# Kernel optimization log

Hardware: AMD Instinct MI355X
Metric: run time of the kernel (lower is better)

## Reference

```python
import jax, jax.numpy as jnp
import numpy as np

B, L, D, H, DFF = 16, 2048, 256, 8, 1024
CYCLES = 2
DEP = D // H
EPS = 1e-6


def _mha(q, k, v, Wq, Wk, Wv, Wo, bo):
    # q: [N, Lq, D], k/v: [N, Lk, D]  (mask is None in the source for both calls)
    N, Lq, _ = q.shape
    Lk = k.shape[1]
    qh = (q @ Wq).reshape(N, Lq, H, DEP)
    kh = (k @ Wk).reshape(N, Lk, H, DEP)
    vh = (v @ Wv).reshape(N, Lk, H, DEP)
    logits = jnp.einsum('nqhd,nkhd->nhqk', qh, kh) / jnp.sqrt(jnp.float32(DEP))
    w = jax.nn.softmax(logits, axis=-1)
    o = jnp.einsum('nhqk,nkhd->nqhd', w, vh).reshape(N, Lq, D)
    return o @ Wo + bo


def _layernorm(x, g, b):
    mu = jnp.mean(x, axis=-1, keepdims=True)
    var = jnp.mean(jnp.square(x - mu), axis=-1, keepdims=True)
    return g * (x - mu) * jax.lax.rsqrt(var + EPS) + b


def setup_inputs() -> dict:
    key = jax.random.key(0)
    ks = jax.random.split(key, 10)
    sc = 1.0 / np.sqrt(D)
    return {
        'e': jax.random.normal(ks[0], (B, L, D), dtype=jnp.float32),
        'Wq': jax.random.normal(ks[1], (D, D), dtype=jnp.float32) * sc,
        'Wk': jax.random.normal(ks[2], (D, D), dtype=jnp.float32) * sc,
        'Wv': jax.random.normal(ks[3], (D, D), dtype=jnp.float32) * sc,
        'Wo': jax.random.normal(ks[4], (D, D), dtype=jnp.float32) * sc,
        'bo': jnp.zeros((D,), dtype=jnp.float32),
        'W1': jax.random.normal(ks[5], (D, DFF), dtype=jnp.float32) * sc,
        'b1': jnp.zeros((DFF,), dtype=jnp.float32),
        'W2': jax.random.normal(ks[6], (DFF, D), dtype=jnp.float32) * (1.0 / np.sqrt(DFF)),
        'b2': jnp.zeros((D,), dtype=jnp.float32),
        'g1': jnp.ones((D,), dtype=jnp.float32),
        'be1': jnp.zeros((D,), dtype=jnp.float32),
        'g2': jnp.ones((D,), dtype=jnp.float32),
        'be2': jnp.zeros((D,), dtype=jnp.float32),
        'training': False,
    }


def reference(e, Wq, Wk, Wv, Wo, bo, W1, b1, W2, b2, g1, be1, g2, be2, training):
    # training=False -> dropouts are identity (eval mode)
    b, l, d = e.shape
    h = e
    s = jnp.mean(h, axis=1)  # relay node [b, d]
    for _ in range(CYCLES):
        h_last = jnp.roll(h, -1, axis=1)  # cycle_shift(h, False)
        h_next = jnp.roll(h, 1, axis=1)   # cycle_shift(h, True)
        s_m = jnp.broadcast_to(s[:, None, :], h.shape)
        # context [b, l, 5, d] -> [b*l, 5, d]
        c = jnp.stack([h_last, h, h_next, e, s_m], axis=-2).reshape(b * l, 5, d)
        hq = h.reshape(b * l, 1, d)
        h = jax.nn.relu(_mha(hq, c, c, Wq, Wk, Wv, Wo, bo)).reshape(b, l, d)
        # relay attention (the source reuses multi_att_satellite weights here)
        sq = s[:, None, :]               # [b, 1, d]
        mc = jnp.concatenate([sq, h], axis=1)  # [b, l+1, d]
        s = jax.nn.relu(_mha(sq, mc, mc, Wq, Wk, Wv, Wo, bo)).reshape(b, d)
    out1 = _layernorm(e + h, g1, be1)
    ffn = jax.nn.relu(out1 @ W1 + b1) @ W2 + b2
    out2 = _layernorm(out1 + ffn, g2, be2)
    return out2, s
```

## Files before the change

kernel.cpp:

```cpp
#include <hip/hip_runtime.h>

typedef unsigned short u16;
typedef unsigned int u32;
typedef __attribute__((ext_vector_type(8))) short bf16x8;
typedef __attribute__((ext_vector_type(4))) float f32x4;

#define LCONST __launch_bounds__(256)

__device__ __forceinline__ u16 f2bf(float f) {
  u32 u = __float_as_uint(f);
  u32 r = (u + 0x7FFFu + ((u >> 16) & 1u)) >> 16;
  return (u16)r;
}
__device__ __forceinline__ float bflo(u32 w) { return __uint_as_float(w << 16); }
__device__ __forceinline__ float bfhi(u32 w) { return __uint_as_float(w & 0xFFFF0000u); }
__device__ __forceinline__ float b2f(u16 v) { return __uint_as_float(((u32)v) << 16); }

__device__ __forceinline__ float dot8(uint4 u, const float* q) {
  return q[0]*bflo(u.x) + q[1]*bfhi(u.x) + q[2]*bflo(u.y) + q[3]*bfhi(u.y)
       + q[4]*bflo(u.z) + q[5]*bfhi(u.z) + q[6]*bflo(u.w) + q[7]*bfhi(u.w);
}
__device__ __forceinline__ void fma8(uint4 u, float wt, float* a) {
  a[0] = fmaf(wt, bflo(u.x), a[0]); a[1] = fmaf(wt, bfhi(u.x), a[1]);
  a[2] = fmaf(wt, bflo(u.y), a[2]); a[3] = fmaf(wt, bfhi(u.y), a[3]);
  a[4] = fmaf(wt, bflo(u.z), a[4]); a[5] = fmaf(wt, bfhi(u.z), a[5]);
  a[6] = fmaf(wt, bflo(u.w), a[6]); a[7] = fmaf(wt, bfhi(u.w), a[7]);
}

__device__ __forceinline__ void gload16(const u16* g, u16* l) {
  __builtin_amdgcn_global_load_lds(
      (const __attribute__((address_space(1))) unsigned int*)g,
      (__attribute__((address_space(3))) unsigned int*)l, 16, 0, 0);
}

__global__ LCONST void prep_kernel(const float* __restrict__ e,
                                   const float* __restrict__ Wq, const float* __restrict__ Wk,
                                   const float* __restrict__ Wv, const float* __restrict__ Wo,
                                   const float* __restrict__ W1, const float* __restrict__ W2,
                                   u16* __restrict__ Wqkv_t, u16* __restrict__ Wo_t,
                                   u16* __restrict__ W1_t, u16* __restrict__ W2_t,
                                   float* __restrict__ part, u16* __restrict__ ebf) {
  int blk = blockIdx.x;
  int tid = threadIdx.x;
  if (blk < 3072) {
    int idx = blk * 256 + tid;
    if (idx < 196608) {
      int sub = idx >> 16, r = idx & 65535;
      int n = r >> 8, k = r & 255;
      const float* src = (sub == 0) ? Wq : ((sub == 1) ? Wk : Wv);
      Wqkv_t[idx] = f2bf(src[(size_t)k * 256 + n]);
    } else if (idx < 262144) {
      int r = idx - 196608;
      int n = r >> 8, k = r & 255;
      Wo_t[r] = f2bf(Wo[(size_t)k * 256 + n]);
    } else if (idx < 524288) {
      int r = idx - 262144;
      int n = r >> 8, k = r & 255;
      W1_t[r] = f2bf(W1[(size_t)k * 1024 + n]);
    } else {
      int r = idx - 524288;
      int n = r >> 10, k = r & 1023;
      W2_t[r] = f2bf(W2[(size_t)k * 256 + n]);
    }
  } else {
    int mb = blk - 3072;
    int b = mb >> 5, c = mb & 31;
    size_t base = ((size_t)b * 2048 + (size_t)c * 64) * 256 + tid;
    float s = 0.f;
    #pragma unroll 8
    for (int i = 0; i < 64; i++) {
      float v = e[base + (size_t)i * 256];
      s += v;
      ebf[base + (size_t)i * 256] = f2bf(v);
    }
    part[(size_t)mb * 256 + tid] = s;
  }
}

template <int BM, int BN, int EPI>
__global__ __launch_bounds__(512, (BM == 128) ? 4 : 6)
void gemm3_kernel(const u16* __restrict__ A, const u16* __restrict__ Bt,
                  const float* __restrict__ bias,
                  u16* __restrict__ C0, u16* __restrict__ C1, u16* __restrict__ C2,
                  const u16* __restrict__ resbf,
                  const float* __restrict__ g, const float* __restrict__ be,
                  float* __restrict__ Fout,
                  int M, int N, int K) {
  constexpr int WR = BM / 2;
  constexpr int MR = WR / 16;
  constexpr int ACH_PW = (BM / 8) / 8;
  constexpr int BCH_PW = 4;
  __shared__ __align__(16) u16 As[BM * 64];
  __shared__ __align__(16) u16 Bs[BN * 64];

  const int tid = threadIdx.x, lane = tid & 63, wid = tid >> 6;
  const int wm = wid >> 2, wn = wid & 3;

  const int ncol = N / BN;
  const int nwg = gridDim.x;
  const int bid = blockIdx.x;
  const int swz = (bid & 7) * (nwg >> 3) + (bid >> 3);
  const int mb = swz / ncol, nb = swz - mb * ncol;
  const int m0 = mb * BM, n0 = nb * BN;

  const int lrow8 = lane >> 3;
  const int cg = (lane & 7) ^ lrow8;

  f32x4 acc[MR][4] = {};
  for (int kt = 0; kt < K; kt += 64) {
    #pragma unroll
    for (int it = 0; it < ACH_PW; it++) {
      int ca = wid * ACH_PW + it;
      int row = ca * 8 + lrow8;
      gload16(A + (size_t)(m0 + row) * K + kt + cg * 8, (u16*)As + ca * 512);
    }
    #pragma unroll
    for (int it = 0; it < BCH_PW; it++) {
      int cb = wid * BCH_PW + it;
      int row = cb * 8 + lrow8;
      gload16(Bt + (size_t)(n0 + row) * K + kt + cg * 8, (u16*)Bs + cb * 512);
    }
    __syncthreads();
    const int lr = lane & 15, hi = lane >> 4;
    #pragma unroll
    for (int kk = 0; kk < 2; kk++) {
      const int slot = (kk * 4 + hi) ^ (lr & 7);
      bf16x8 af[MR], bfr[4];
      #pragma unroll
      for (int m = 0; m < MR; m++)
        af[m] = *(const bf16x8*)&As[(wm * WR + m * 16 + lr) * 64 + slot * 8];
      #pragma unroll
      for (int n = 0; n < 4; n++)
        bfr[n] = *(const bf16x8*)&Bs[(wn * 64 + n * 16 + lr) * 64 + slot * 8];
      #pragma unroll
      for (int m = 0; m < MR; m++)
        #pragma unroll
        for (int n = 0; n < 4; n++)
          acc[m][n] = __builtin_amdgcn_mfma_f32_16x16x32_bf16(af[m], bfr[n], acc[m][n], 0, 0, 0);
    }
    __syncthreads();
  }

  const int lr = lane & 15, hi = lane >> 4;
  if constexpr (EPI == 0) {
    const int bsel = n0 >> 8;
    u16* C = (bsel == 0) ? C0 : ((bsel == 1) ? C1 : C2);
    #pragma unroll
    for (int m = 0; m < MR; m++)
      #pragma unroll
      for (int n = 0; n < 4; n++)
        #pragma unroll
        for (int r = 0; r < 4; r++) {
          int row = m0 + wm * WR + m * 16 + hi * 4 + r;
          int col = wn * 64 + n * 16 + lr;
          C[(size_t)row * 256 + col] = f2bf(acc[m][n][r]);
        }
  } else if constexpr (EPI == 1) {
    #pragma unroll
    for (int m = 0; m < MR; m++)
      #pragma unroll
      for (int n = 0; n < 4; n++)
        #pragma unroll
        for (int r = 0; r < 4; r++) {
          int row = m0 + wm * WR + m * 16 + hi * 4 + r;
          int col = n0 + wn * 64 + n * 16 + lr;
          float v = fmaxf(acc[m][n][r] + bias[col], 0.f);
          C0[(size_t)row * N + col] = f2bf(v);
        }
  } else {
    __shared__ float rsum[BM], rsq[BM];
    if (tid < BM) { rsum[tid] = 0.f; rsq[tid] = 0.f; }
    __syncthreads();
    #pragma unroll
    for (int m = 0; m < MR; m++)
      #pragma unroll
      for (int n = 0; n < 4; n++)
        #pragma unroll
        for (int r = 0; r < 4; r++) {
          int rl = wm * WR + m * 16 + hi * 4 + r;
          int col = wn * 64 + n * 16 + lr;
          size_t gi = (size_t)(m0 + rl) * 256 + col;
          acc[m][n][r] = acc[m][n][r] + bias[col] + b2f(resbf[gi]);
        }
    #pragma unroll
    for (int m = 0; m < MR; m++)
      #pragma unroll
      for (int r = 0; r < 4; r++) {
        float s = 0.f, q = 0.f;
        #pragma unroll
        for (int n = 0; n < 4; n++) { float x = acc[m][n][r]; s += x; q += x * x; }
        #pragma unroll
        for (int off = 1; off < 16; off <<= 1) {
          s += __shfl_xor(s, off);
          q += __shfl_xor(q, off);
        }
        if (lr == 0) {
          int rl = wm * WR + m * 16 + hi * 4 + r;
          atomicAdd(&rsum[rl], s);
          atomicAdd(&rsq[rl], q);
        }
      }
    __syncthreads();
    #pragma unroll
    for (int m = 0; m < MR; m++)
      #pragma unroll
      for (int n = 0; n < 4; n++)
        #pragma unroll
        for (int r = 0; r < 4; r++) {
          int rl = wm * WR + m * 16 + hi * 4 + r;
          int col = wn * 64 + n * 16 + lr;
          size_t gi = (size_t)(m0 + rl) * 256 + col;
          float mu = rsum[rl] * (1.f / 256.f);
          float var = rsq[rl] * (1.f / 256.f) - mu * mu;
          float rstd = rsqrtf(fmaxf(var, 0.f) + 1e-6f);
          Fout[gi] = g[col] * (acc[m][n][r] - mu) * rstd + be[col];
        }
  }
}

template <int EPI>
__global__ __launch_bounds__(512, 4)
void attnwo_kernel(const u16* __restrict__ hq, const u16* __restrict__ pk,
                   const u16* __restrict__ pv, const u16* __restrict__ ek,
                   const u16* __restrict__ ev, const float* __restrict__ skp,
                   const float* __restrict__ svp,
                   const u16* __restrict__ Wo_t, const float* __restrict__ bo,
                   u16* __restrict__ C0, u16* __restrict__ C1,
                   const u16* __restrict__ resbf,
                   const float* __restrict__ g, const float* __restrict__ be) {
  __shared__ __align__(16) u16 As[64 * 256];
  __shared__ __align__(16) u16 Bs[256 * 64];
  const int tid = threadIdx.x, lane = tid & 63, wid = tid >> 6;
  const int wm = wid >> 2, wn = wid & 3;
  const int nwg = gridDim.x, bid = blockIdx.x;
  const int swz = (bid & 7) * (nwg >> 3) + (bid >> 3);
  const int m0 = swz * 64;

  {
    const int r = tid >> 3, h = tid & 7;
    const size_t token = (size_t)(m0 + r);
    const int b = (int)(token >> 11);
    const int i = (int)(token & 2047);
    const size_t tb = (size_t)b << 11;
    const size_t ip = tb + ((i + 1) & 2047);
    const size_t im = tb + ((i + 2047) & 2047);
    const int off = h * 32;

    float qf[32];
    {
      const u16* q = hq + token * 256 + off;
      #pragma unroll
      for (int c = 0; c < 4; c++) {
        uint4 u = *(const uint4*)(q + c * 8);
        qf[c*8+0] = bflo(u.x); qf[c*8+1] = bfhi(u.x);
        qf[c*8+2] = bflo(u.y); qf[c*8+3] = bfhi(u.y);
        qf[c*8+4] = bflo(u.z); qf[c*8+5] = bfhi(u.z);
        qf[c*8+6] = bflo(u.w); qf[c*8+7] = bfhi(u.w);
      }
    }
    const u16* kr0 = pk + ip * 256 + off;
    const u16* kr1 = pk + token * 256 + off;
    const u16* kr2 = pk + im * 256 + off;
    const u16* kr3 = ek + token * 256 + off;
    float lg[5];
    {
      float d0 = 0, d1 = 0, d2 = 0, d3 = 0;
      #pragma unroll
      for (int cc = 0; cc < 4; cc++) {
        d0 += dot8(*(const uint4*)(kr0 + cc * 8), qf + cc * 8);
        d1 += dot8(*(const uint4*)(kr1 + cc * 8), qf + cc * 8);
        d2 += dot8(*(const uint4*)(kr2 + cc * 8), qf + cc * 8);
        d3 += dot8(*(const uint4*)(kr3 + cc * 8), qf + cc * 8);
      }
      lg[0] = d0; lg[1] = d1; lg[2] = d2; lg[3] = d3;
      float d4 = 0;
      const float* s = skp + b * 256 + off;
      #pragma unroll
      for (int j = 0; j < 32; j++) d4 = fmaf(qf[j], s[j], d4);
      lg[4] = d4;
    }
    const float sc = 0.17677669529663687f;
    float mx = lg[0];
    #pragma unroll
    for (int c = 1; c < 5; c++) mx = fmaxf(mx, lg[c]);
    float w[5], den = 0.f;
    #pragma unroll
    for (int c = 0; c < 5; c++) { w[c] = __expf((lg[c] - mx) * sc); den += w[c]; }

    float a[32];
    #pragma unroll
    for (int j = 0; j < 32; j++) a[j] = 0.f;
    const u16* vr0 = pv + ip * 256 + off;
    const u16* vr1 = pv + token * 256 + off;
    const u16* vr2 = pv + im * 256 + off;
    const u16* vr3 = ev + token * 256 + off;
    #pragma unroll
    for (int cc = 0; cc < 4; cc++) {
      fma8(*(const uint4*)(vr0 + cc * 8), w[0], a + cc * 8);
      fma8(*(const uint4*)(vr1 + cc * 8), w[1], a + cc * 8);
      fma8(*(const uint4*)(vr2 + cc * 8), w[2], a + cc * 8);
      fma8(*(const uint4*)(vr3 + cc * 8), w[3], a + cc * 8);
    }
    {
      const float* s = svp + b * 256 + off;
      #pragma unroll
      for (int j = 0; j < 32; j++) a[j] = fmaf(w[4], s[j], a[j]);
    }
    const float inv = 1.f / den;
    #pragma unroll
    for (int c = 0; c < 4; c++) {
      uint4 u;
      u.x = (u32)f2bf(a[c*8+0] * inv) | ((u32)f2bf(a[c*8+1] * inv) << 16);
      u.y = (u32)f2bf(a[c*8+2] * inv) | ((u32)f2bf(a[c*8+3] * inv) << 16);
      u.z = (u32)f2bf(a[c*8+4] * inv) | ((u32)f2bf(a[c*8+5] * inv) << 16);
      u.w = (u32)f2bf(a[c*8+6] * inv) | ((u32)f2bf(a[c*8+7] * inv) << 16);
      int s = h * 4 + c;
      int sp = (s & 24) | ((s & 7) ^ (r & 7));
      *(uint4*)&As[r * 256 + sp * 8] = u;
    }
  }
  __syncthreads();

  const int lrow8 = lane >> 3;
  const int cg = (lane & 7) ^ lrow8;
  const int lr = lane & 15, hi = lane >> 4;
  f32x4 acc[2][4] = {};
  for (int kt = 0; kt < 4; kt++) {
    #pragma unroll
    for (int it = 0; it < 4; it++) {
      int cb = wid * 4 + it;
      int row = cb * 8 + lrow8;
      gload16(Wo_t + (size_t)row * 256 + kt * 64 + cg * 8, (u16*)Bs + cb * 512);
    }
    __syncthreads();
    #pragma unroll
    for (int kk = 0; kk < 2; kk++) {
      bf16x8 af[2], bfr[4];
      #pragma unroll
      for (int m = 0; m < 2; m++) {
        int row = wm * 32 + m * 16 + lr;
        int sp = kt * 8 + ((kk * 4 + hi) ^ (row & 7));
        af[m] = *(const bf16x8*)&As[row * 256 + sp * 8];
      }
      const int slotB = (kk * 4 + hi) ^ (lr & 7);
      #pragma unroll
      for (int n = 0; n < 4; n++)
        bfr[n] = *(const bf16x8*)&Bs[(wn * 64 + n * 16 + lr) * 64 + slotB * 8];
      #pragma unroll
      for (int m = 0; m < 2; m++)
        #pragma unroll
        for (int n = 0; n < 4; n++)
          acc[m][n] = __builtin_amdgcn_mfma_f32_16x16x32_bf16(af[m], bfr[n], acc[m][n], 0, 0, 0);
    }
    __syncthreads();
  }

  if constexpr (EPI == 1) {
    #pragma unroll
    for (int m = 0; m < 2; m++)
      #pragma unroll
      for (int n = 0; n < 4; n++)
        #pragma unroll
        for (int r = 0; r < 4; r++) {
          int row = m0 + wm * 32 + m * 16 + hi * 4 + r;
          int col = wn * 64 + n * 16 + lr;
          float v = fmaxf(acc[m][n][r] + bo[col], 0.f);
          C0[(size_t)row * 256 + col] = f2bf(v);
        }
  } else {
    __shared__ float rsum[64], rsq[64];
    if (tid < 64) { rsum[tid] = 0.f; rsq[tid] = 0.f; }
    __syncthreads();
    #pragma unroll
    for (int m = 0; m < 2; m++)
      #pragma unroll
      for (int n = 0; n < 4; n++)
        #pragma unroll
        for (int r = 0; r < 4; r++) {
          int rl = wm * 32 + m * 16 + hi * 4 + r;
          int col = wn * 64 + n * 16 + lr;
          size_t gi = (size_t)(m0 + rl) * 256 + col;
          float v = fmaxf(acc[m][n][r] + bo[col], 0.f);
          C0[gi] = f2bf(v);
          acc[m][n][r] = b2f(resbf[gi]) + v;
        }
    #pragma unroll
    for (int m = 0; m < 2; m++)
      #pragma unroll
      for (int r = 0; r < 4; r++) {
        float s = 0.f, q = 0.f;
        #pragma unroll
        for (int n = 0; n < 4; n++) { float x = acc[m][n][r]; s += x; q += x * x; }
        #pragma unroll
        for (int off = 1; off < 16; off <<= 1) {
          s += __shfl_xor(s, off);
          q += __shfl_xor(q, off);
        }
        if (lr == 0) {
          int rl = wm * 32 + m * 16 + hi * 4 + r;
          atomicAdd(&rsum[rl], s);
          atomicAdd(&rsq[rl], q);
        }
      }
    __syncthreads();
    #pragma unroll
    for (int m = 0; m < 2; m++)
      #pragma unroll
      for (int n = 0; n < 4; n++)
        #pragma unroll
        for (int r = 0; r < 4; r++) {
          int rl = wm * 32 + m * 16 + hi * 4 + r;
          int col = wn * 64 + n * 16 + lr;
          size_t gi = (size_t)(m0 + rl) * 256 + col;
          float mu = rsum[rl] * (1.f / 256.f);
          float var = rsq[rl] * (1.f / 256.f) - mu * mu;
          float rstd = rsqrtf(fmaxf(var, 0.f) + 1e-6f);
          C1[gi] = f2bf(g[col] * (acc[m][n][r] - mu) * rstd + be[col]);
        }
  }
}

template <bool MEAN>
__global__ LCONST void proj_kernel(const float* __restrict__ X, const float* __restrict__ part,
                                   const float* __restrict__ Wq, const float* __restrict__ Wk,
                                   const float* __restrict__ Wv, float* __restrict__ Yq,
                                   float* __restrict__ Yk, float* __restrict__ Yv) {
  __shared__ float xs[256];
  __shared__ float red[256];
  const int b = blockIdx.x;
  const int wsel = blockIdx.y >> 2, n0 = (blockIdx.y & 3) * 64;
  const int tid = threadIdx.x;
  if constexpr (MEAN) {
    float s = 0.f;
    #pragma unroll
    for (int c = 0; c < 32; c++) s += part[((size_t)b * 32 + c) * 256 + tid];
    xs[tid] = s * (1.f / 2048.f);
  } else {
    xs[tid] = X[b * 256 + tid];
  }
  __syncthreads();
  const float* W = (wsel == 0) ? Wq : ((wsel == 1) ? Wk : Wv);
  float* Y = (wsel == 0) ? Yq : ((wsel == 1) ? Yk : Yv);
  const int c = tid & 63, g = tid >> 6;
  float p = 0.f;
  #pragma unroll 8
  for (int j = g * 64; j < g * 64 + 64; j++)
    p = fmaf(xs[j], W[(size_t)j * 256 + n0 + c], p);
  red[tid] = p;
  __syncthreads();
  if (g == 0)
    Y[b * 256 + n0 + c] = red[c] + red[64 + c] + red[128 + c] + red[192 + c];
}

__global__ LCONST void mha2a_kernel(const float* __restrict__ sqp, const float* __restrict__ skp,
                                    const float* __restrict__ svp, const u16* __restrict__ pk,
                                    const u16* __restrict__ pv, float* __restrict__ partial) {
  __shared__ float rmax[4], rsum[4], racc[4][32];
  const int blk = blockIdx.x;
  const int bh = blk >> 2, c = blk & 3;
  const int b = bh >> 3, h = bh & 7;
  const int tid = threadIdx.x;
  const int lane = tid & 63, wid = tid >> 6;
  const int off = h * 32;
  const float sc = 0.17677669529663687f;

  float qf[32];
  {
    const float* q = sqp + b * 256 + off;
    #pragma unroll
    for (int j = 0; j < 32; j++) qf[j] = q[j];
  }
  const int k0 = c * 512 + tid;
  const int k1 = k0 + 256;
  const u16* kp0 = pk + ((size_t)b * 2048 + k0) * 256 + off;
  const u16* kp1 = pk + ((size_t)b * 2048 + k1) * 256 + off;
  float d0 = 0.f, d1 = 0.f;
  #pragma unroll
  for (int cc = 0; cc < 4; cc++) {
    d0 += dot8(*(const uint4*)(kp0 + cc * 8), qf + cc * 8);
    d1 += dot8(*(const uint4*)(kp1 + cc * 8), qf + cc * 8);
  }
  d0 *= sc; d1 *= sc;
  float ds = -1e30f;
  if (c == 0 && tid == 0) {
    float d = 0.f;
    const float* k = skp + b * 256 + off;
    #pragma unroll
    for (int j = 0; j < 32; j++) d = fmaf(qf[j], k[j], d);
    ds = d * sc;
  }
  float lmax = fmaxf(fmaxf(d0, d1), ds);
  #pragma unroll
  for (int o = 32; o; o >>= 1) lmax = fmaxf(lmax, __shfl_down(lmax, o));
  if (lane == 0) rmax[wid] = lmax;
  __syncthreads();
  const float M = fmaxf(fmaxf(rmax[0], rmax[1]), fmaxf(rmax[2], rmax[3]));

  float w0 = __expf(d0 - M), w1 = __expf(d1 - M);
  float lsum = w0 + w1;
  float a[32];
  #pragma unroll
  for (int j = 0; j < 32; j++) a[j] = 0.f;
  const u16* vp0 = pv + ((size_t)b * 2048 + k0) * 256 + off;
  const u16* vp1 = pv + ((size_t)b * 2048 + k1) * 256 + off;
  #pragma unroll
  for (int cc = 0; cc < 4; cc++) {
    fma8(*(const uint4*)(vp0 + cc * 8), w0, a + cc * 8);
    fma8(*(const uint4*)(vp1 + cc * 8), w1, a + cc * 8);
  }
  if (c == 0 && tid == 0) {
    float ws = __expf(ds - M);
    lsum += ws;
    const float* v = svp + b * 256 + off;
    #pragma unroll
    for (int j = 0; j < 32; j++) a[j] = fmaf(ws, v[j], a[j]);
  }
  #pragma unroll
  for (int o = 32; o; o >>= 1) lsum += __shfl_down(lsum, o);
  if (lane == 0) rsum[wid] = lsum;
  #pragma unroll
  for (int j = 0; j < 32; j++) {
    float v = a[j];
    #pragma unroll
    for (int o = 32; o; o >>= 1) v += __shfl_down(v, o);
    if (lane == 0) racc[wid][j] = v;
  }
  __syncthreads();
  float* P = partial + (size_t)blk * 36;
  if (tid < 32) {
    P[2 + tid] = racc[0][tid] + racc[1][tid] + racc[2][tid] + racc[3][tid];
    if (tid == 0) {
      P[0] = M;
      P[1] = rsum[0] + rsum[1] + rsum[2] + rsum[3];
    }
  }
}

__global__ LCONST void mha2c_kernel(const float* __restrict__ partial,
                                    const float* __restrict__ Wo, const float* __restrict__ bo,
                                    float* __restrict__ Y) {
  __shared__ float xs[256];
  __shared__ float red[256];
  const int b = blockIdx.x;
  const int n0 = blockIdx.y * 64;
  const int tid = threadIdx.x;
  {
    int hh = tid >> 5, d = tid & 31;
    const float* P = partial + (size_t)(b * 8 + hh) * 144;
    float M = fmaxf(fmaxf(P[0], P[36]), fmaxf(P[72], P[108]));
    float l = 0.f, o = 0.f;
    #pragma unroll
    for (int c = 0; c < 4; c++) {
      float f = __expf(P[c * 36] - M);
      l += f * P[c * 36 + 1];
      o += f * P[c * 36 + 2 + d];
    }
    xs[tid] = o / l;
  }
  __syncthreads();
  const int c = tid & 63, g = tid >> 6;
  float p = 0.f;
  #pragma unroll 8
  for (int j = g * 64; j < g * 64 + 64; j++)
    p = fmaf(xs[j], Wo[(size_t)j * 256 + n0 + c], p);
  red[tid] = p;
  __syncthreads();
  if (g == 0) {
    float v = red[c] + red[64 + c] + red[128 + c] + red[192 + c];
    Y[b * 256 + n0 + c] = fmaxf(v + bo[n0 + c], 0.f);
  }
}

extern "C" void kernel_launch(void* const* d_in, const int* in_sizes, int n_in,
                              void* d_out, int out_size, void* d_ws, size_t ws_size,
                              hipStream_t stream) {
  const float* e   = (const float*)d_in[0];
  const float* Wq  = (const float*)d_in[1];
  const float* Wk  = (const float*)d_in[2];
  const float* Wv  = (const float*)d_in[3];
  const float* Wo  = (const float*)d_in[4];
  const float* bo  = (const float*)d_in[5];
  const float* W1  = (const float*)d_in[6];
  const float* b1  = (const float*)d_in[7];
  const float* W2  = (const float*)d_in[8];
  const float* b2  = (const float*)d_in[9];
  const float* g1  = (const float*)d_in[10];
  const float* be1 = (const float*)d_in[11];
  const float* g2  = (const float*)d_in[12];
  const float* be2 = (const float*)d_in[13];

  char* wsb = (char*)d_ws;
  size_t off = 0;
  auto alc = [&](size_t n) { void* p = wsb + off; off += (n + 255) & ~(size_t)255; return p; };
  u16* Wqkv_t = (u16*)alc(768 * 256 * 2);
  u16* Wo_t   = (u16*)alc(65536 * 2);
  u16* W1_t   = (u16*)alc(262144 * 2);
  u16* W2_t   = (u16*)alc(262144 * 2);
  float* sB    = (float*)alc(4096 * 4);
  float* sqp   = (float*)alc(4096 * 4);
  float* skp   = (float*)alc(4096 * 4);
  float* svp   = (float*)alc(4096 * 4);
  float* partM = (float*)alc(512 * 36 * 4);
  float* part  = (float*)alc(524288);
  const size_t SZ = 16777216;
  u16* hq   = (u16*)alc(SZ);
  u16* ek   = (u16*)alc(SZ);
  u16* ev   = (u16*)alc(SZ);
  u16* pk   = (u16*)alc(SZ);
  u16* pv   = (u16*)alc(SZ);
  u16* hbuf = (u16*)alc(SZ);
  u16* ebf  = (u16*)alc(SZ);
  u16* out1 = (u16*)alc(SZ);
  u16* ffn1 = hq;

  const int M = 32768;
  float* outp  = (float*)d_out;
  float* s_out = outp + 8388608;

  prep_kernel<<<3584, 256, 0, stream>>>(e, Wq, Wk, Wv, Wo, W1, W2,
      Wqkv_t, Wo_t, W1_t, W2_t, part, ebf);

  proj_kernel<true><<<dim3(16, 12), 256, 0, stream>>>(nullptr, part, Wq, Wk, Wv, sqp, skp, svp);
  gemm3_kernel<128, 256, 0><<<768, 512, 0, stream>>>(ebf, Wqkv_t, nullptr, hq, ek, ev,
      nullptr, nullptr, nullptr, nullptr, M, 768, 256);
  attnwo_kernel<1><<<512, 512, 0, stream>>>(hq, ek, ev, ek, ev, skp, svp,
      Wo_t, bo, hbuf, nullptr, nullptr, nullptr, nullptr);
  gemm3_kernel<128, 256, 0><<<768, 512, 0, stream>>>(hbuf, Wqkv_t, nullptr, hq, pk, pv,
      nullptr, nullptr, nullptr, nullptr, M, 768, 256);
  mha2a_kernel<<<512, 256, 0, stream>>>(sqp, skp, svp, pk, pv, partM);
  mha2c_kernel<<<dim3(16, 4), 256, 0, stream>>>(partM, Wo, bo, sB);
  proj_kernel<false><<<dim3(16, 12), 256, 0, stream>>>(sB, nullptr, Wq, Wk, Wv, sqp, skp, svp);

  attnwo_kernel<2><<<512, 512, 0, stream>>>(hq, pk, pv, ek, ev, skp, svp,
      Wo_t, bo, hbuf, out1, ebf, g1, be1);
  gemm3_kernel<128, 256, 0><<<512, 512, 0, stream>>>(hbuf, Wqkv_t + 65536, nullptr, pk, pv, nullptr,
      nullptr, nullptr, nullptr, nullptr, M, 512, 256);
  mha2a_kernel<<<512, 256, 0, stream>>>(sqp, skp, svp, pk, pv, partM);
  mha2c_kernel<<<dim3(16, 4), 256, 0, stream>>>(partM, Wo, bo, s_out);

  gemm3_kernel<128, 256, 1><<<1024, 512, 0, stream>>>(out1, W1_t, b1, ffn1, nullptr, nullptr,
      nullptr, nullptr, nullptr, nullptr, M, 1024, 256);
  gemm3_kernel<64, 256, 4><<<512, 512, 0, stream>>>(ffn1, W2_t, b2, nullptr, nullptr, nullptr,
      out1, g2, be2, outp, M, 256, 1024);
  (void)in_sizes; (void)n_in; (void)out_size; (void)ws_size;
}
```

Baseline: 258.5 us.

## Merge independent GEMM and attention launches into horizontally fused kernels

Measured after the change: 262.8 us. About the same (+1.7%).

```diff
diff --git a/kernel.cpp b/kernel.cpp
--- a/kernel.cpp
+++ b/kernel.cpp
@@ -78,7 +78,144 @@
 }
 
 template <int BM, int BN, int EPI>
-__global__ __launch_bounds__(512, (BM == 128) ? 4 : 6)
+__device__ __forceinline__ void gemm_core(
+    int bid, int nwg, u16* As, u16* Bs,
+    const u16* __restrict__ A, const u16* __restrict__ Bt,
+    const float* __restrict__ bias,
+    u16* __restrict__ C0, u16* __restrict__ C1, u16* __restrict__ C2,
+    const u16* __restrict__ resbf,
+    const float* __restrict__ g, const float* __restrict__ be,
+    float* __restrict__ Fout, int N, int K) {
+  constexpr int WR = BM / 2;
+  constexpr int MR = WR / 16;
+  constexpr int ACH_PW = (BM / 8) / 8;
+  constexpr int BCH_PW = 4;
+
+  const int tid = threadIdx.x, lane = tid & 63, wid = tid >> 6;
+  const int wm = wid >> 2, wn = wid & 3;
+
+  const int ncol = N / BN;
+  const int swz = (bid & 7) * (nwg >> 3) + (bid >> 3);
+  const int mb = swz / ncol, nb = swz - mb * ncol;
+  const int m0 = mb * BM, n0 = nb * BN;
+
+  const int lrow8 = lane >> 3;
+  const int cg = (lane & 7) ^ lrow8;
+
+  f32x4 acc[MR][4] = {};
+  for (int kt = 0; kt < K; kt += 64) {
+    #pragma unroll
+    for (int it = 0; it < ACH_PW; it++) {
+      int ca = wid * ACH_PW + it;
+      int row = ca * 8 + lrow8;
+      gload16(A + (size_t)(m0 + row) * K + kt + cg * 8, As + ca * 512);
+    }
+    #pragma unroll
+    for (int it = 0; it < BCH_PW; it++) {
+      int cb = wid * BCH_PW + it;
+      int row = cb * 8 + lrow8;
+      gload16(Bt + (size_t)(n0 + row) * K + kt + cg * 8, Bs + cb * 512);
+    }
+    __syncthreads();
+    const int lr = lane & 15, hi = lane >> 4;
+    #pragma unroll
+    for (int kk = 0; kk < 2; kk++) {
+      const int slot = (kk * 4 + hi) ^ (lr & 7);
+      bf16x8 af[MR], bfr[4];
+      #pragma unroll
+      for (int m = 0; m < MR; m++)
+        af[m] = *(const bf16x8*)&As[(wm * WR + m * 16 + lr) * 64 + slot * 8];
+      #pragma unroll
+      for (int n = 0; n < 4; n++)
+        bfr[n] = *(const bf16x8*)&Bs[(wn * 64 + n * 16 + lr) * 64 + slot * 8];
+      #pragma unroll
+      for (int m = 0; m < MR; m++)
+        #pragma unroll
+        for (int n = 0; n < 4; n++)
+          acc[m][n] = __builtin_amdgcn_mfma_f32_16x16x32_bf16(af[m], bfr[n], acc[m][n], 0, 0, 0);
+    }
+    __syncthreads();
+  }
+
+  const int lr = lane & 15, hi = lane >> 4;
+  if constexpr (EPI == 0) {
+    const int bsel = n0 >> 8;
+    u16* C = (bsel == 0) ? C0 : ((bsel == 1) ? C1 : C2);
+    #pragma unroll
+    for (int m = 0; m < MR; m++)
+      #pragma unroll
+      for (int n = 0; n < 4; n++)
+        #pragma unroll
+        for (int r = 0; r < 4; r++) {
+          int row = m0 + wm * WR + m * 16 + hi * 4 + r;
+          int col = wn * 64 + n * 16 + lr;
+          C[(size_t)row * 256 + col] = f2bf(acc[m][n][r]);
+        }
+  } else if constexpr (EPI == 1) {
+    #pragma unroll
+    for (int m = 0; m < MR; m++)
+      #pragma unroll
+      for (int n = 0; n < 4; n++)
+        #pragma unroll
+        for (int r = 0; r < 4; r++) {
+          int row = m0 + wm * WR + m * 16 + hi * 4 + r;
+          int col = n0 + wn * 64 + n * 16 + lr;
+          float v = fmaxf(acc[m][n][r] + bias[col], 0.f);
+          C0[(size_t)row * N + col] = f2bf(v);
+        }
+  } else {
+    __shared__ float rs_[BM], rq_[BM];
+    if (tid < BM) { rs_[tid] = 0.f; rq_[tid] = 0.f; }
+    __syncthreads();
+    #pragma unroll
+    for (int m = 0; m < MR; m++)
+      #pragma unroll
+      for (int n = 0; n < 4; n++)
+        #pragma unroll
+        for (int r = 0; r < 4; r++) {
+          int rl = wm * WR + m * 16 + hi * 4 + r;
+          int col = wn * 64 + n * 16 + lr;
+          size_t gi = (size_t)(m0 + rl) * 256 + col;
+          acc[m][n][r] = acc[m][n][r] + bias[col] + b2f(resbf[gi]);
+        }
+    #pragma unroll
+    for (int m = 0; m < MR; m++)
+      #pragma unroll
+      for (int r = 0; r < 4; r++) {
+        float s = 0.f, q = 0.f;
+        #pragma unroll
+        for (int n = 0; n < 4; n++) { float x = acc[m][n][r]; s += x; q += x * x; }
+        #pragma unroll
+        for (int off = 1; off < 16; off <<= 1) {
+          s += __shfl_xor(s, off);
+          q += __shfl_xor(q, off);
+        }
+        if (lr == 0) {
+          int rl = wm * WR + m * 16 + hi * 4 + r;
+          atomicAdd(&rs_[rl], s);
+          atomicAdd(&rq_[rl], q);
+        }
+      }
+    __syncthreads();
+    #pragma unroll
+    for (int m = 0; m < MR; m++)
+      #pragma unroll
+      for (int n = 0; n < 4; n++)
+        #pragma unroll
+        for (int r = 0; r < 4; r++) {
+          int rl = wm * WR + m * 16 + hi * 4 + r;
+          int col = wn * 64 + n * 16 + lr;
+          size_t gi = (size_t)(m0 + rl) * 256 + col;
+          float mu = rs_[rl] * (1.f / 256.f);
+          float var = rq_[rl] * (1.f / 256.f) - mu * mu;
+          float rstd = rsqrtf(fmaxf(var, 0.f) + 1e-6f);
+          Fout[gi] = g[col] * (acc[m][n][r] - mu) * rstd + be[col];
+        }
+  }
+}
+
+template <int BM, int BN, int EPI>
+__global__ __launch_bounds__(512, 4)
 void gemm3_kernel(const u16* __restrict__ A, const u16* __restrict__ Bt,
                   const float* __restrict__ bias,
                   u16* __restrict__ C0, u16* __restrict__ C1, u16* __restrict__ C2,
@@ -86,136 +223,114 @@
                   const float* __restrict__ g, const float* __restrict__ be,
                   float* __restrict__ Fout,
                   int M, int N, int K) {
-  constexpr int WR = BM / 2;
-  constexpr int MR = WR / 16;
-  constexpr int ACH_PW = (BM / 8) / 8;
-  constexpr int BCH_PW = 4;
   __shared__ __align__(16) u16 As[BM * 64];
   __shared__ __align__(16) u16 Bs[BN * 64];
-
-  const int tid = threadIdx.x, lane = tid & 63, wid = tid >> 6;
-  const int wm = wid >> 2, wn = wid & 3;
-
-  const int ncol = N / BN;
-  const int nwg = gridDim.x;
-  const int bid = blockIdx.x;
-  const int swz = (bid & 7) * (nwg >> 3) + (bid >> 3);
-  const int mb = swz / ncol, nb = swz - mb * ncol;
-  const int m0 = mb * BM, n0 = nb * BN;
-
-  const int lrow8 = lane >> 3;
-  const int cg = (lane & 7) ^ lrow8;
-
-  f32x4 acc[MR][4] = {};
-  for (int kt = 0; kt < K; kt += 64) {
-    #pragma unroll
-    for (int it = 0; it < ACH_PW; it++) {
-      int ca = wid * ACH_PW + it;
-      int row = ca * 8 + lrow8;
-      gload16(A + (size_t)(m0 + row) * K + kt + cg * 8, (u16*)As + ca * 512);
-    }
-    #pragma unroll
-    for (int it = 0; it < BCH_PW; it++) {
-      int cb = wid * BCH_PW + it;
-      int row = cb * 8 + lrow8;
-      gload16(Bt + (size_t)(n0 + row) * K + kt + cg * 8, (u16*)Bs + cb * 512);
-    }
-    __syncthreads();
-    const int lr = lane & 15, hi = lane >> 4;
-    #pragma unroll
-    for (int kk = 0; kk < 2; kk++) {
-      const int slot = (kk * 4 + hi) ^ (lr & 7);
-      bf16x8 af[MR], bfr[4];
-      #pragma unroll
-      for (int m = 0; m < MR; m++)
-        af[m] = *(const bf16x8*)&As[(wm * WR + m * 16 + lr) * 64 + slot * 8];
-      #pragma unroll
-      for (int n = 0; n < 4; n++)
-        bfr[n] = *(const bf16x8*)&Bs[(wn * 64 + n * 16 + lr) * 64 + slot * 8];
-      #pragma unroll
-      for (int m = 0; m < MR; m++)
-        #pragma unroll
-        for (int n = 0; n < 4; n++)
-          acc[m][n] = __builtin_amdgcn_mfma_f32_16x16x32_bf16(af[m], bfr[n], acc[m][n], 0, 0, 0);
-    }
-    __syncthreads();
-  }
-
-  const int lr = lane & 15, hi = lane >> 4;
-  if constexpr (EPI == 0) {
-    const int bsel = n0 >> 8;
-    u16* C = (bsel == 0) ? C0 : ((bsel == 1) ? C1 : C2);
-    #pragma unroll
-    for (int m = 0; m < MR; m++)
-      #pragma unroll
-      for (int n = 0; n < 4; n++)
-        #pragma unroll
-        for (int r = 0; r < 4; r++) {
-          int row = m0 + wm * WR + m * 16 + hi * 4 + r;
-          int col = wn * 64 + n * 16 + lr;
-          C[(size_t)row * 256 + col] = f2bf(acc[m][n][r]);
-        }
-  } else if constexpr (EPI == 1) {
-    #pragma unroll
-    for (int m = 0; m < MR; m++)
-      #pragma unroll
-      for (int n = 0; n < 4; n++)
-        #pragma unroll
-        for (int r = 0; r < 4; r++) {
-          int row = m0 + wm * WR + m * 16 + hi * 4 + r;
-          int col = n0 + wn * 64 + n * 16 + lr;
-          float v = fmaxf(acc[m][n][r] + bias[col], 0.f);
-          C0[(size_t)row * N + col] = f2bf(v);
-        }
-  } else {
-    __shared__ float rsum[BM], rsq[BM];
-    if (tid < BM) { rsum[tid] = 0.f; rsq[tid] = 0.f; }
-    __syncthreads();
-    #pragma unroll
-    for (int m = 0; m < MR; m++)
-      #pragma unroll
-      for (int n = 0; n < 4; n++)
-        #pragma unroll
-        for (int r = 0; r < 4; r++) {
-          int rl = wm * WR + m * 16 + hi * 4 + r;
-          int col = wn * 64 + n * 16 + lr;
-          size_t gi = (size_t)(m0 + rl) * 256 + col;
-          acc[m][n][r] = acc[m][n][r] + bias[col] + b2f(resbf[gi]);
-        }
-    #pragma unroll
-    for (int m = 0; m < MR; m++)
-      #pragma unroll
-      for (int r = 0; r < 4; r++) {
-        float s = 0.f, q = 0.f;
-        #pragma unroll
-        for (int n = 0; n < 4; n++) { float x = acc[m][n][r]; s += x; q += x * x; }
-        #pragma unroll
-        for (int off = 1; off < 16; off <<= 1) {
-          s += __shfl_xor(s, off);
-          q += __shfl_xor(q, off);
-        }
-        if (lr == 0) {
-          int rl = wm * WR + m * 16 + hi * 4 + r;
-          atomicAdd(&rsum[rl], s);
-          atomicAdd(&rsq[rl], q);
-        }
-      }
-    __syncthreads();
-    #pragma unroll
-    for (int m = 0; m < MR; m++)
-      #pragma unroll
-      for (int n = 0; n < 4; n++)
-        #pragma unroll
-        for (int r = 0; r < 4; r++) {
-          int rl = wm * WR + m * 16 + hi * 4 + r;
-          int col = wn * 64 + n * 16 + lr;
-          size_t gi = (size_t)(m0 + rl) * 256 + col;
-          float mu = rsum[rl] * (1.f / 256.f);
-          float var = rsq[rl] * (1.f / 256.f) - mu * mu;
-          float rstd = rsqrtf(fmaxf(var, 0.f) + 1e-6f);
-          Fout[gi] = g[col] * (acc[m][n][r] - mu) * rstd + be[col];
-        }
-  }
+  gemm_core<BM, BN, EPI>(blockIdx.x, gridDim.x, As, Bs, A, Bt, bias,
+                         C0, C1, C2, resbf, g, be, Fout, N, K);
+  (void)M;
+}
+
+template <int NT>
+__device__ __forceinline__ void mha2a_body(int blk,
+    const float* __restrict__ sqp, const float* __restrict__ skp,
+    const float* __restrict__ svp, const u16* __restrict__ pk,
+    const u16* __restrict__ pv, float* __restrict__ partial) {
+  constexpr int NW = NT / 64;
+  constexpr int KPT = 512 / NT;
+  __shared__ float rmax[NW], rsm[NW], racc[NW][32];
+  const int bh = blk >> 2, c = blk & 3;
+  const int b = bh >> 3, h = bh & 7;
+  const int tid = threadIdx.x;
+  const int lane = tid & 63, wid = tid >> 6;
+  const int off = h * 32;
+  const float sc = 0.17677669529663687f;
+
+  float qf[32];
+  {
+    const float* q = sqp + b * 256 + off;
+    #pragma unroll
+    for (int j = 0; j < 32; j++) qf[j] = q[j];
+  }
+  float d[KPT];
+  #pragma unroll
+  for (int kk = 0; kk < KPT; kk++) {
+    int k = c * 512 + kk * NT + tid;
+    const u16* kp = pk + ((size_t)b * 2048 + k) * 256 + off;
+    float dv = 0.f;
+    #pragma unroll
+    for (int cc = 0; cc < 4; cc++) dv += dot8(*(const uint4*)(kp + cc * 8), qf + cc * 8);
+    d[kk] = dv * sc;
+  }
+  float ds = -1e30f;
+  if (c == 0 && tid == 0) {
+    float dv = 0.f;
+    const float* k = skp + b * 256 + off;
+    #pragma unroll
+    for (int j = 0; j < 32; j++) dv = fmaf(qf[j], k[j], dv);
+    ds = dv * sc;
+  }
+  float lmax = ds;
+  #pragma unroll
+  for (int kk = 0; kk < KPT; kk++) lmax = fmaxf(lmax, d[kk]);
+  #pragma unroll
+  for (int o = 32; o; o >>= 1) lmax = fmaxf(lmax, __shfl_down(lmax, o));
+  if (lane == 0) rmax[wid] = lmax;
+  __syncthreads();
+  float M = rmax[0];
+  #pragma unroll
+  for (int w = 1; w < NW; w++) M = fmaxf(M, rmax[w]);
+
+  float lsum = 0.f;
+  float a[32];
+  #pragma unroll
+  for (int j = 0; j < 32; j++) a[j] = 0.f;
+  #pragma unroll
+  for (int kk = 0; kk < KPT; kk++) {
+    int k = c * 512 + kk * NT + tid;
+    float wt = __expf(d[kk] - M);
+    lsum += wt;
+    const u16* vp = pv + ((size_t)b * 2048 + k) * 256 + off;
+    #pragma unroll
+    for (int cc = 0; cc < 4; cc++) fma8(*(const uint4*)(vp + cc * 8), wt, a + cc * 8);
+  }
+  if (c == 0 && tid == 0) {
+    float ws = __expf(ds - M);
+    lsum += ws;
+    const float* v = svp + b * 256 + off;
+    #pragma unroll
+    for (int j = 0; j < 32; j++) a[j] = fmaf(ws, v[j], a[j]);
+  }
+  #pragma unroll
+  for (int o = 32; o; o >>= 1) lsum += __shfl_down(lsum, o);
+  if (lane == 0) rsm[wid] = lsum;
+  #pragma unroll
+  for (int j = 0; j < 32; j++) {
+    float v = a[j];
+    #pragma unroll
+    for (int o = 32; o; o >>= 1) v += __shfl_down(v, o);
+    if (lane == 0) racc[wid][j] = v;
+  }
+  __syncthreads();
+  float* P = partial + (size_t)blk * 36;
+  if (tid < 32) {
+    float acc = 0.f;
+    #pragma unroll
+    for (int w = 0; w < NW; w++) acc += racc[w][tid];
+    P[2 + tid] = acc;
+    if (tid == 0) {
+      float l = 0.f;
+      #pragma unroll
+      for (int w = 0; w < NW; w++) l += rsm[w];
+      P[0] = M;
+      P[1] = l;
+    }
+  }
+}
+
+__global__ LCONST void mha2a_kernel(const float* __restrict__ sqp, const float* __restrict__ skp,
+                                    const float* __restrict__ svp, const u16* __restrict__ pk,
+                                    const u16* __restrict__ pv, float* __restrict__ partial) {
+  mha2a_body<256>(blockIdx.x, sqp, skp, svp, pk, pv, partial);
 }
 
 template <int EPI>
@@ -235,6 +350,15 @@
   const int nwg = gridDim.x, bid = blockIdx.x;
   const int swz = (bid & 7) * (nwg >> 3) + (bid >> 3);
   const int m0 = swz * 64;
+  const int lrow8 = lane >> 3;
+  const int cg = (lane & 7) ^ lrow8;
+
+  #pragma unroll
+  for (int it = 0; it < 4; it++) {
+    int cb = wid * 4 + it;
+    int row = cb * 8 + lrow8;
+    gload16(Wo_t + (size_t)row * 256 + 0 * 64 + cg * 8, (u16*)Bs + cb * 512);
+  }
 
   {
     const int r = tid >> 3, h = tid & 7;
@@ -321,18 +445,9 @@
   }
   __syncthreads();
 
-  const int lrow8 = lane >> 3;
-  const int cg = (lane & 7) ^ lrow8;
   const int lr = lane & 15, hi = lane >> 4;
   f32x4 acc[2][4] = {};
   for (int kt = 0; kt < 4; kt++) {
-    #pragma unroll
-    for (int it = 0; it < 4; it++) {
-      int cb = wid * 4 + it;
-      int row = cb * 8 + lrow8;
-      gload16(Wo_t + (size_t)row * 256 + kt * 64 + cg * 8, (u16*)Bs + cb * 512);
-    }
-    __syncthreads();
     #pragma unroll
     for (int kk = 0; kk < 2; kk++) {
       bf16x8 af[2], bfr[4];
@@ -353,6 +468,15 @@
           acc[m][n] = __builtin_amdgcn_mfma_f32_16x16x32_bf16(af[m], bfr[n], acc[m][n], 0, 0, 0);
     }
     __syncthreads();
+    if (kt < 3) {
+      #pragma unroll
+      for (int it = 0; it < 4; it++) {
+        int cb = wid * 4 + it;
+        int row = cb * 8 + lrow8;
+        gload16(Wo_t + (size_t)row * 256 + (kt + 1) * 64 + cg * 8, (u16*)Bs + cb * 512);
+      }
+      __syncthreads();
+    }
   }
 
   if constexpr (EPI == 1) {
@@ -452,87 +576,86 @@
     Y[b * 256 + n0 + c] = red[c] + red[64 + c] + red[128 + c] + red[192 + c];
 }
 
-__global__ LCONST void mha2a_kernel(const float* __restrict__ sqp, const float* __restrict__ skp,
-                                    const float* __restrict__ svp, const u16* __restrict__ pk,
-                                    const u16* __restrict__ pv, float* __restrict__ partial) {
-  __shared__ float rmax[4], rsum[4], racc[4][32];
-  const int blk = blockIdx.x;
-  const int bh = blk >> 2, c = blk & 3;
-  const int b = bh >> 3, h = bh & 7;
-  const int tid = threadIdx.x;
-  const int lane = tid & 63, wid = tid >> 6;
-  const int off = h * 32;
-  const float sc = 0.17677669529663687f;
-
-  float qf[32];
-  {
-    const float* q = sqp + b * 256 + off;
-    #pragma unroll
-    for (int j = 0; j < 32; j++) qf[j] = q[j];
-  }
-  const int k0 = c * 512 + tid;
-  const int k1 = k0 + 256;
-  const u16* kp0 = pk + ((size_t)b * 2048 + k0) * 256 + off;
-  const u16* kp1 = pk + ((size_t)b * 2048 + k1) * 256 + off;
-  float d0 = 0.f, d1 = 0.f;
-  #pragma unroll
-  for (int cc = 0; cc < 4; cc++) {
-    d0 += dot8(*(const uint4*)(kp0 + cc * 8), qf + cc * 8);
-    d1 += dot8(*(const uint4*)(kp1 + cc * 8), qf + cc * 8);
-  }
-  d0 *= sc; d1 *= sc;
-  float ds = -1e30f;
-  if (c == 0 && tid == 0) {
-    float d = 0.f;
-    const float* k = skp + b * 256 + off;
-    #pragma unroll
-    for (int j = 0; j < 32; j++) d = fmaf(qf[j], k[j], d);
-    ds = d * sc;
-  }
-  float lmax = fmaxf(fmaxf(d0, d1), ds);
-  #pragma unroll
-  for (int o = 32; o; o >>= 1) lmax = fmaxf(lmax, __shfl_down(lmax, o));
-  if (lane == 0) rmax[wid] = lmax;
-  __syncthreads();
-  const float M = fmaxf(fmaxf(rmax[0], rmax[1]), fmaxf(rmax[2], rmax[3]));
-
-  float w0 = __expf(d0 - M), w1 = __expf(d1 - M);
-  float lsum = w0 + w1;
-  float a[32];
-  #pragma unroll
-  for (int j = 0; j < 32; j++) a[j] = 0.f;
-  const u16* vp0 = pv + ((size_t)b * 2048 + k0) * 256 + off;
-  const u16* vp1 = pv + ((size_t)b * 2048 + k1) * 256 + off;
-  #pragma unroll
-  for (int cc = 0; cc < 4; cc++) {
-    fma8(*(const uint4*)(vp0 + cc * 8), w0, a + cc * 8);
-    fma8(*(const uint4*)(vp1 + cc * 8), w1, a + cc * 8);
-  }
-  if (c == 0 && tid == 0) {
-    float ws = __expf(ds - M);
-    lsum += ws;
-    const float* v = svp + b * 256 + off;
-    #pragma unroll
-    for (int j = 0; j < 32; j++) a[j] = fmaf(ws, v[j], a[j]);
-  }
-  #pragma unroll
-  for (int o = 32; o; o >>= 1) lsum += __shfl_down(lsum, o);
-  if (lane == 0) rsum[wid] = lsum;
-  #pragma unroll
-  for (int j = 0; j < 32; j++) {
-    float v = a[j];
-    #pragma unroll
-    for (int o = 32; o; o >>= 1) v += __shfl_down(v, o);
-    if (lane == 0) racc[wid][j] = v;
-  }
-  __syncthreads();
-  float* P = partial + (size_t)blk * 36;
-  if (tid < 32) {
-    P[2 + tid] = racc[0][tid] + racc[1][tid] + racc[2][tid] + racc[3][tid];
-    if (tid == 0) {
-      P[0] = M;
-      P[1] = rsum[0] + rsum[1] + rsum[2] + rsum[3];
-    }
+__global__ __launch_bounds__(512, 4)
+void qkvproj_kernel(const u16* __restrict__ ebf, const u16* __restrict__ Wqkv_t,
+                    u16* __restrict__ hq, u16* __restrict__ ek, u16* __restrict__ ev,
+                    const float* __restrict__ part,
+                    const float* __restrict__ Wq, const float* __restrict__ Wk,
+                    const float* __restrict__ Wv, float* __restrict__ Yq,
+                    float* __restrict__ Yk, float* __restrict__ Yv) {
+  extern __shared__ __align__(16) char smem[];
+  const int bid = blockIdx.x, tid = threadIdx.x;
+  if (bid < 768) {
+    u16* As = (u16*)smem;
+    u16* Bs = As + 128 * 64;
+    gemm_core<128, 256, 0>(bid, 768, As, Bs, ebf, Wqkv_t, nullptr,
+                           hq, ek, ev, nullptr, nullptr, nullptr, nullptr, 768, 256);
+  } else {
+    float* xs = (float*)smem;
+    float* red = xs + 256;
+    const int vb = bid - 768;
+    const int b = vb & 15, y = vb >> 4;
+    const int wsel = y >> 2, n0 = (y & 3) * 64;
+    if (tid < 256) {
+      float s = 0.f;
+      #pragma unroll
+      for (int c = 0; c < 32; c++) s += part[((size_t)b * 32 + c) * 256 + tid];
+      xs[tid] = s * (1.f / 2048.f);
+    }
+    __syncthreads();
+    const float* W = (wsel == 0) ? Wq : ((wsel == 1) ? Wk : Wv);
+    float* Y = (wsel == 0) ? Yq : ((wsel == 1) ? Yk : Yv);
+    const int c = tid & 63, g = tid >> 6;
+    float p = 0.f;
+    #pragma unroll 8
+    for (int j = g * 32; j < g * 32 + 32; j++)
+      p = fmaf(xs[j], W[(size_t)j * 256 + n0 + c], p);
+    red[tid] = p;
+    __syncthreads();
+    if (g == 0) {
+      float v = 0.f;
+      #pragma unroll
+      for (int k = 0; k < 8; k++) v += red[k * 64 + c];
+      Y[b * 256 + n0 + c] = v;
+    }
+  }
+}
+
+__global__ __launch_bounds__(512, 4)
+void kvffn_kernel(const u16* __restrict__ out1, const u16* __restrict__ W1_t,
+                  const float* __restrict__ b1, u16* __restrict__ ffn1,
+                  const u16* __restrict__ hbuf, const u16* __restrict__ Wkv_t,
+                  u16* __restrict__ pk, u16* __restrict__ pv) {
+  extern __shared__ __align__(16) char smem[];
+  u16* As = (u16*)smem;
+  u16* Bs = As + 128 * 64;
+  const int bid = blockIdx.x;
+  if (bid < 1024) {
+    gemm_core<128, 256, 1>(bid, 1024, As, Bs, out1, W1_t, b1,
+                           ffn1, nullptr, nullptr, nullptr, nullptr, nullptr, nullptr, 1024, 256);
+  } else {
+    gemm_core<128, 256, 0>(bid - 1024, 512, As, Bs, hbuf, Wkv_t, nullptr,
+                           pk, pv, nullptr, nullptr, nullptr, nullptr, nullptr, 512, 256);
+  }
+}
+
+__global__ __launch_bounds__(512, 4)
+void ffn2mha_kernel(const u16* __restrict__ ffn1, const u16* __restrict__ W2_t,
+                    const float* __restrict__ b2, const u16* __restrict__ out1,
+                    const float* __restrict__ g2, const float* __restrict__ be2,
+                    float* __restrict__ outp,
+                    const float* __restrict__ sqp, const float* __restrict__ skp,
+                    const float* __restrict__ svp, const u16* __restrict__ pk,
+                    const u16* __restrict__ pv, float* __restrict__ partial) {
+  extern __shared__ __align__(16) char smem[];
+  const int bid = blockIdx.x;
+  if (bid < 512) {
+    u16* As = (u16*)smem;
+    u16* Bs = As + 64 * 64;
+    gemm_core<64, 256, 4>(bid, 512, As, Bs, ffn1, W2_t, b2,
+                          nullptr, nullptr, nullptr, out1, g2, be2, outp, 256, 1024);
+  } else {
+    mha2a_body<512>(bid - 512, sqp, skp, svp, pk, pv, partial);
   }
 }
 
@@ -606,10 +729,10 @@
   u16* hq   = (u16*)alc(SZ);
   u16* ek   = (u16*)alc(SZ);
   u16* ev   = (u16*)alc(SZ);
+  u16* ebf  = (u16*)alc(SZ);
   u16* pk   = (u16*)alc(SZ);
   u16* pv   = (u16*)alc(SZ);
   u16* hbuf = (u16*)alc(SZ);
-  u16* ebf  = (u16*)alc(SZ);
   u16* out1 = (u16*)alc(SZ);
   u16* ffn1 = hq;
 
@@ -620,9 +743,8 @@
   prep_kernel<<<3584, 256, 0, stream>>>(e, Wq, Wk, Wv, Wo, W1, W2,
       Wqkv_t, Wo_t, W1_t, W2_t, part, ebf);
 
-  proj_kernel<true><<<dim3(16, 12), 256, 0, stream>>>(nullptr, part, Wq, Wk, Wv, sqp, skp, svp);
-  gemm3_kernel<128, 256, 0><<<768, 512, 0, stream>>>(ebf, Wqkv_t, nullptr, hq, ek, ev,
-      nullptr, nullptr, nullptr, nullptr, M, 768, 256);
+  qkvproj_kernel<<<960, 512, 49152, stream>>>(ebf, Wqkv_t, hq, ek, ev,
+      part, Wq, Wk, Wv, sqp, skp, svp);
   attnwo_kernel<1><<<512, 512, 0, stream>>>(hq, ek, ev, ek, ev, skp, svp,
       Wo_t, bo, hbuf, nullptr, nullptr, nullptr, nullptr);
   gemm3_kernel<128, 256, 0><<<768, 512, 0, stream>>>(hbuf, Wqkv_t, nullptr, hq, pk, pv,
@@ -633,14 +755,10 @@
 
   attnwo_kernel<2><<<512, 512, 0, stream>>>(hq, pk, pv, ek, ev, skp, svp,
       Wo_t, bo, hbuf, out1, ebf, g1, be1);
-  gemm3_kernel<128, 256, 0><<<512, 512, 0, stream>>>(hbuf, Wqkv_t + 65536, nullptr, pk, pv, nullptr,
-      nullptr, nullptr, nullptr, nullptr, M, 512, 256);
-  mha2a_kernel<<<512, 256, 0, stream>>>(sqp, skp, svp, pk, pv, partM);
+  kvffn_kernel<<<1536, 512, 49152, stream>>>(out1, W1_t, b1, ffn1,
+      hbuf, Wqkv_t + 65536, pk, pv);
+  ffn2mha_kernel<<<1024, 512, 40960, stream>>>(ffn1, W2_t, b2, out1, g2, be2, outp,
+      sqp, skp, svp, pk, pv, partM);
   mha2c_kernel<<<dim3(16, 4), 256, 0, stream>>>(partM, Wo, bo, s_out);
-
-  gemm3_kernel<128, 256, 1><<<1024, 512, 0, stream>>>(out1, W1_t, b1, ffn1, nullptr, nullptr,
-      nullptr, nullptr, nullptr, nullptr, M, 1024, 256);
-  gemm3_kernel<64, 256, 4><<<512, 512, 0, stream>>>(ffn1, W2_t, b2, nullptr, nullptr, nullptr,
-      out1, g2, be2, outp, M, 256, 1024);
   (void)in_sizes; (void)n_in; (void)out_size; (void)ws_size;
 }
```
